# Performance work log

Hardware: AMD Instinct MI355X
Metric: run time of the kernel (lower is better)

Reference implementation:

```python
import jax, jax.numpy as jnp
import numpy as np

N = 20000      # nodes
E = 320000     # edges (before self-loops)
G = 64         # graphs in batch
H = 4          # attention heads
C = 64         # channels per head
HID = H * C    # 256
IN = 128       # input feature dim
LAT = 64       # latent dim
NEG = 0.2      # LeakyReLU negative slope (PyG GATConv default)
BN_EPS = 1e-5
N_LAYERS = 3


def setup_inputs() -> dict:
    key = jax.random.key(0)
    ks = jax.random.split(key, 24)
    s = 0.1
    return dict(
        x=jax.random.normal(ks[0], (N, IN), jnp.float32),
        edge_index=jax.random.randint(ks[1], (2, E), 0, N, dtype=jnp.int32),
        batch=jnp.sort(jax.random.randint(ks[2], (N,), 0, G, dtype=jnp.int32)),
        W0=jax.random.normal(ks[3], (IN, HID), jnp.float32) * s,
        W_rest=jax.random.normal(ks[4], (N_LAYERS - 1, HID, HID), jnp.float32) * s,
        att_src=jax.random.normal(ks[5], (N_LAYERS, H, C), jnp.float32) * s,
        att_dst=jax.random.normal(ks[6], (N_LAYERS, H, C), jnp.float32) * s,
        bias_conv=jax.random.normal(ks[7], (N_LAYERS, HID), jnp.float32) * s,
        bn_gamma=jax.random.uniform(ks[8], (N_LAYERS, HID), jnp.float32) + 0.5,
        bn_beta=jax.random.normal(ks[9], (N_LAYERS, HID), jnp.float32) * s,
        bn_mean=jax.random.normal(ks[10], (N_LAYERS, HID), jnp.float32) * s,
        bn_var=jax.random.uniform(ks[11], (N_LAYERS, HID), jnp.float32) + 0.5,
        lbn_gamma=jax.random.uniform(ks[12], (HID,), jnp.float32) + 0.5,
        lbn_beta=jax.random.normal(ks[13], (HID,), jnp.float32) * s,
        lbn_mean=jax.random.normal(ks[14], (HID,), jnp.float32) * s,
        lbn_var=jax.random.uniform(ks[15], (HID,), jnp.float32) + 0.5,
        fc_W=jax.random.normal(ks[16], (HID, LAT), jnp.float32) * s,
        fc_b=jax.random.normal(ks[17], (LAT,), jnp.float32) * s,
    )


def _gat_layer(x, src, dst, W, a_src, a_dst, bias):
    # linear transform -> [N, H, C]
    xp = (x @ W).reshape(N, H, C)
    # per-node attention scalars [N, H]
    al_s = (xp * a_src).sum(-1)
    al_d = (xp * a_dst).sum(-1)
    # per-edge logit for edge j->i: leaky_relu(a_s[j] + a_d[i])
    e = jax.nn.leaky_relu(al_s[src] + al_d[dst], NEG)  # [E', H]
    # softmax over incoming edges of each target node
    emax = jax.ops.segment_max(e, dst, num_segments=N)  # [N, H]
    ex = jnp.exp(e - emax[dst])
    denom = jax.ops.segment_sum(ex, dst, num_segments=N)
    alpha = ex / (denom[dst] + 1e-16)
    # weighted scatter-add of source features
    msg = xp[src] * alpha[:, :, None]                    # [E', H, C]
    out = jax.ops.segment_sum(msg, dst, num_segments=N)  # [N, H, C]
    return out.reshape(N, HID) + bias


def _bn_eval(x, gamma, beta, mean, var):
    return (x - mean) * jax.lax.rsqrt(var + BN_EPS) * gamma + beta


def reference(x, edge_index, batch, W0, W_rest, att_src, att_dst, bias_conv,
              bn_gamma, bn_beta, bn_mean, bn_var,
              lbn_gamma, lbn_beta, lbn_mean, lbn_var, fc_W, fc_b):
    # PyG convention: edge_index[0]=source, edge_index[1]=target; GATConv adds self-loops
    loop = jnp.arange(N, dtype=edge_index.dtype)
    src = jnp.concatenate([edge_index[0], loop])
    dst = jnp.concatenate([edge_index[1], loop])
    h = x
    for i in range(N_LAYERS):
        W = W0 if i == 0 else W_rest[i - 1]
        h = _gat_layer(h, src, dst, W, att_src[i], att_dst[i], bias_conv[i])
        h = _bn_eval(h, bn_gamma[i], bn_beta[i], bn_mean[i], bn_var[i])
        h = jax.nn.relu(h)
        # dropout is identity in eval mode
    pooled = jax.ops.segment_sum(h, batch, num_segments=G)  # [G, HID]
    pooled = _bn_eval(pooled, lbn_gamma, lbn_beta, lbn_mean, lbn_var)
    return pooled @ fc_W + fc_b  # [G, LAT]
```

## Files before the change

kernel.cpp:

```cpp
#include <hip/hip_runtime.h>
#include <hip/hip_bf16.h>
#include <cmath>

#define NN   20000
#define NE   320000
#define EE   (NE + NN)
#define NG   64
#define NH   4
#define NC   64
#define HIDD 256
#define IND  128
#define LATD 64
#define NEGS 0.2f
#define BNEPS 1e-5f
#define MPAD 20096
#define PSPLIT 16
#define NB   ((NN + 255) / 256)

#define BM 128
#define BN 64
#define BK 64

typedef __attribute__((ext_vector_type(8))) short short8;
typedef __attribute__((ext_vector_type(4))) float f32x4;

__device__ inline int lower_bound_i(const int* __restrict__ b, int n, int key) {
    int lo = 0, hi = n;
    while (lo < hi) { int mid = (lo + hi) >> 1; if (b[mid] < key) lo = mid + 1; else hi = mid; }
    return lo;
}

__device__ inline float sel4(float4 v, int h) {
    float r = v.x;
    r = (h == 1) ? v.y : r;
    r = (h == 2) ? v.z : r;
    r = (h == 3) ? v.w : r;
    return r;
}

__device__ inline float bf2f(unsigned short u) {
    return __uint_as_float(((unsigned int)u) << 16);
}

__global__ void k_zero(int* __restrict__ p, int n) {
    int i = blockIdx.x * blockDim.x + threadIdx.x;
    if (i < n) p[i] = 0;
}

__global__ void k_cast_x(const float* __restrict__ x, __hip_bfloat16* __restrict__ hbx) {
    int i = blockIdx.x * blockDim.x + threadIdx.x;
    if (i >= NN * IND / 4) return;
    float4 v = ((const float4*)x)[i];
    union { __hip_bfloat16 b[4]; ushort4 u; } cv;
    cv.b[0] = __float2bfloat16(v.x); cv.b[1] = __float2bfloat16(v.y);
    cv.b[2] = __float2bfloat16(v.z); cv.b[3] = __float2bfloat16(v.w);
    ((ushort4*)hbx)[i] = cv.u;
}

__global__ void k_cast_wt_all(const float* __restrict__ W0, const float* __restrict__ Wr,
                              __hip_bfloat16* __restrict__ Wt3) {
    int k = blockIdx.x;
    int l = blockIdx.y;
    int n = threadIdx.x;
    int K = (l == 0) ? IND : HIDD;
    if (k >= K) return;
    const float* W = (l == 0) ? W0 : (Wr + (size_t)(l - 1) * HIDD * HIDD);
    size_t off = (l == 0) ? 0 : ((size_t)HIDD * IND + (size_t)(l - 1) * HIDD * HIDD);
    Wt3[off + (size_t)n * K + k] = __float2bfloat16(W[(size_t)k * HIDD + n]);
}

__global__ void k_hist(const int* __restrict__ ei, int* __restrict__ deg) {
    int e = blockIdx.x * blockDim.x + threadIdx.x;
    if (e >= EE) return;
    int d = (e < NE) ? ei[NE + e] : (e - NE);
    atomicAdd(&deg[d], 1);
}

__global__ __launch_bounds__(256) void k_blocksum(const int* __restrict__ deg,
                                                  int* __restrict__ bsum) {
    __shared__ int s[256];
    int i = blockIdx.x * 256 + threadIdx.x;
    s[threadIdx.x] = (i < NN) ? deg[i] : 0;
    __syncthreads();
    for (int off = 128; off > 0; off >>= 1) {
        if (threadIdx.x < off) s[threadIdx.x] += s[threadIdx.x + off];
        __syncthreads();
    }
    if (threadIdx.x == 0) bsum[blockIdx.x] = s[0];
}

__global__ __launch_bounds__(128) void k_scanbs(const int* __restrict__ bsum,
                                                int* __restrict__ boff,
                                                int* __restrict__ row_ptr) {
    __shared__ int s[128];
    int tid = threadIdx.x;
    int v = (tid < NB) ? bsum[tid] : 0;
    s[tid] = v;
    __syncthreads();
    for (int off = 1; off < 128; off <<= 1) {
        int t = (tid >= off) ? s[tid - off] : 0;
        __syncthreads();
        s[tid] += t;
        __syncthreads();
    }
    if (tid < NB) boff[tid] = s[tid] - v;
    if (tid == NB - 1) row_ptr[NN] = s[tid];
}

__global__ __launch_bounds__(256) void k_scanapply(const int* __restrict__ deg,
                                                   const int* __restrict__ boff,
                                                   int* __restrict__ row_ptr,
                                                   int* __restrict__ cursor) {
    __shared__ int s[256];
    int i = blockIdx.x * 256 + threadIdx.x;
    int v = (i < NN) ? deg[i] : 0;
    s[threadIdx.x] = v;
    __syncthreads();
    for (int off = 1; off < 256; off <<= 1) {
        int t = (threadIdx.x >= off) ? s[threadIdx.x - off] : 0;
        __syncthreads();
        s[threadIdx.x] += t;
        __syncthreads();
    }
    if (i < NN) {
        int excl = boff[blockIdx.x] + s[threadIdx.x] - v;
        row_ptr[i] = excl; cursor[i] = excl;
    }
}

__global__ void k_csr_scatter(const int* __restrict__ ei, int* __restrict__ cursor,
                              int* __restrict__ col_idx) {
    int e = blockIdx.x * blockDim.x + threadIdx.x;
    if (e >= EE) return;
    int s, d;
    if (e < NE) { s = ei[e]; d = ei[NE + e]; } else { s = d = e - NE; }
    int pos = atomicAdd(&cursor[d], 1);
    col_idx[pos] = s;
}

__global__ __launch_bounds__(256) void k_gemm(const short* __restrict__ A,
                                              const short* __restrict__ Bt,
                                              int K, __hip_bfloat16* __restrict__ Cb,
                                              const float* __restrict__ a_src,
                                              const float* __restrict__ a_dst,
                                              float* __restrict__ al_s,
                                              float* __restrict__ al_d) {
    __shared__ char As[BM * BK * 2];
    __shared__ char Bs[BN * BK * 2];
    __shared__ float redS[2][BM];
    __shared__ float redD[2][BM];
    int tid = threadIdx.x;
    int lane = tid & 63;
    int wid = tid >> 6;
    int wm = wid >> 1, wn = wid & 1;
    int bm0 = blockIdx.x * BM, bn0 = blockIdx.y * BN;
    int r16 = lane & 15, kg = lane >> 4;

    f32x4 acc[4][2];
    #pragma unroll
    for (int m = 0; m < 4; ++m)
        #pragma unroll
        for (int n = 0; n < 2; ++n) acc[m][n] = (f32x4){0.f, 0.f, 0.f, 0.f};

    for (int k0 = 0; k0 < K; k0 += BK) {
        __syncthreads();
        #pragma unroll
        for (int p = 0; p < 4; ++p) {
            int row = p * 32 + (tid >> 3);
            int cg  = tid & 7;
            uint4 v = *(const uint4*)(A + (size_t)(bm0 + row) * K + k0 + cg * 8);
            *(uint4*)(As + row * 128 + ((cg * 16) ^ ((row & 7) << 4))) = v;
        }
        #pragma unroll
        for (int p = 0; p < 2; ++p) {
            int row = p * 32 + (tid >> 3);
            int cg  = tid & 7;
            uint4 v = *(const uint4*)(Bt + (size_t)(bn0 + row) * K + k0 + cg * 8);
            *(uint4*)(Bs + row * 128 + ((cg * 16) ^ ((row & 7) << 4))) = v;
        }
        __syncthreads();
        #pragma unroll
        for (int kk = 0; kk < 2; ++kk) {
            short8 af[4], bfr[2];
            int kb = (kk * 32 + kg * 8) * 2;
            #pragma unroll
            for (int m = 0; m < 4; ++m) {
                int row = wm * 64 + m * 16 + r16;
                af[m] = *(const short8*)(As + row * 128 + (kb ^ ((row & 7) << 4)));
            }
            #pragma unroll
            for (int n = 0; n < 2; ++n) {
                int row = wn * 32 + n * 16 + r16;
                bfr[n] = *(const short8*)(Bs + row * 128 + (kb ^ ((row & 7) << 4)));
            }
            #pragma unroll
            for (int m = 0; m < 4; ++m)
                #pragma unroll
                for (int n = 0; n < 2; ++n)
                    acc[m][n] = __builtin_amdgcn_mfma_f32_16x16x32_bf16(af[m], bfr[n], acc[m][n], 0, 0, 0);
        }
    }

    #pragma unroll
    for (int m = 0; m < 4; ++m) {
        int row = bm0 + wm * 64 + m * 16 + kg * 4;
        #pragma unroll
        for (int n = 0; n < 2; ++n) {
            int col = bn0 + wn * 32 + n * 16 + r16;
            #pragma unroll
            for (int r = 0; r < 4; ++r)
                Cb[(size_t)(row + r) * HIDD + col] = __float2bfloat16(acc[m][n][r]);
        }
    }

    int headbase = bn0;
    float as0 = a_src[headbase + wn * 32 + r16];
    float as1 = a_src[headbase + wn * 32 + 16 + r16];
    float ad0 = a_dst[headbase + wn * 32 + r16];
    float ad1 = a_dst[headbase + wn * 32 + 16 + r16];
    #pragma unroll
    for (int m = 0; m < 4; ++m) {
        #pragma unroll
        for (int r = 0; r < 4; ++r) {
            float ps = as0 * acc[m][0][r] + as1 * acc[m][1][r];
            float pd = ad0 * acc[m][0][r] + ad1 * acc[m][1][r];
            #pragma unroll
            for (int msk = 1; msk < 16; msk <<= 1) {
                ps += __shfl_xor(ps, msk, 64);
                pd += __shfl_xor(pd, msk, 64);
            }
            if (r16 == 0) {
                int rl = wm * 64 + m * 16 + kg * 4 + r;
                redS[wn][rl] = ps;
                redD[wn][rl] = pd;
            }
        }
    }
    __syncthreads();
    if (tid < BM) {
        int node = bm0 + tid;
        al_s[node * NH + blockIdx.y] = redS[0][tid] + redS[1][tid];
        al_d[node * NH + blockIdx.y] = redD[0][tid] + redD[1][tid];
    }
}

#define EDGE_BODY(I) \
    { float l = as##I + adh; l = l > 0.f ? l : NEGS * l; \
      float wt = __expf(l); den##I += wt; \
      acc##I.x = fmaf(wt, bf2f(xv##I.x), acc##I.x); \
      acc##I.y = fmaf(wt, bf2f(xv##I.y), acc##I.y); \
      acc##I.z = fmaf(wt, bf2f(xv##I.z), acc##I.z); \
      acc##I.w = fmaf(wt, bf2f(xv##I.w), acc##I.w); }

__global__ __launch_bounds__(256) void k_gat_agg(
        const int* __restrict__ row_ptr, const int* __restrict__ col_idx,
        const float* __restrict__ al_s, const float* __restrict__ al_d,
        const __hip_bfloat16* __restrict__ xpb,
        const float* __restrict__ bias, const float* __restrict__ bg,
        const float* __restrict__ bb, const float* __restrict__ bm,
        const float* __restrict__ bv,
        float* __restrict__ h, __hip_bfloat16* __restrict__ hb, int wmask) {
    int wid = threadIdx.x >> 6, lane = threadIdx.x & 63;
    int node = blockIdx.x * 4 + wid;
    if (node >= NN) return;
    int lo = row_ptr[node], hi = row_ptr[node + 1];
    int hsel = lane >> 4;
    float adh = sel4(((const float4*)al_d)[node], hsel);

    float4 acc0 = {0,0,0,0}, acc1 = {0,0,0,0}, acc2 = {0,0,0,0}, acc3 = {0,0,0,0};
    float den0 = 0.f, den1 = 0.f, den2 = 0.f, den3 = 0.f;

    int e = lo;
    for (; e + 3 < hi; e += 4) {
        int sc0 = col_idx[e], sc1 = col_idx[e + 1], sc2 = col_idx[e + 2], sc3 = col_idx[e + 3];
        float as0 = al_s[sc0 * NH + hsel];
        float as1 = al_s[sc1 * NH + hsel];
        float as2 = al_s[sc2 * NH + hsel];
        float as3 = al_s[sc3 * NH + hsel];
        ushort4 xv0 = ((const ushort4*)(xpb + (size_t)sc0 * HIDD))[lane];
        ushort4 xv1 = ((const ushort4*)(xpb + (size_t)sc1 * HIDD))[lane];
        ushort4 xv2 = ((const ushort4*)(xpb + (size_t)sc2 * HIDD))[lane];
        ushort4 xv3 = ((const ushort4*)(xpb + (size_t)sc3 * HIDD))[lane];
        EDGE_BODY(0) EDGE_BODY(1) EDGE_BODY(2) EDGE_BODY(3)
    }
    for (; e < hi; ++e) {
        int sc0 = col_idx[e];
        float as0 = al_s[sc0 * NH + hsel];
        ushort4 xv0 = ((const ushort4*)(xpb + (size_t)sc0 * HIDD))[lane];
        EDGE_BODY(0)
    }

    float den = (den0 + den1) + (den2 + den3);
    float inv = 1.f / (den + 1e-16f);
    float4 acc;
    acc.x = ((acc0.x + acc1.x) + (acc2.x + acc3.x)) * inv;
    acc.y = ((acc0.y + acc1.y) + (acc2.y + acc3.y)) * inv;
    acc.z = ((acc0.z + acc1.z) + (acc2.z + acc3.z)) * inv;
    acc.w = ((acc0.w + acc1.w) + (acc2.w + acc3.w)) * inv;

    float4 bi = ((const float4*)bias)[lane];
    float4 gg = ((const float4*)bg)[lane];
    float4 be = ((const float4*)bb)[lane];
    float4 mn = ((const float4*)bm)[lane];
    float4 vr = ((const float4*)bv)[lane];
    float4 val;
    val.x = (acc.x + bi.x - mn.x) * rsqrtf(vr.x + BNEPS) * gg.x + be.x;
    val.y = (acc.y + bi.y - mn.y) * rsqrtf(vr.y + BNEPS) * gg.y + be.y;
    val.z = (acc.z + bi.z - mn.z) * rsqrtf(vr.z + BNEPS) * gg.z + be.z;
    val.w = (acc.w + bi.w - mn.w) * rsqrtf(vr.w + BNEPS) * gg.w + be.w;
    val.x = val.x > 0.f ? val.x : 0.f;
    val.y = val.y > 0.f ? val.y : 0.f;
    val.z = val.z > 0.f ? val.z : 0.f;
    val.w = val.w > 0.f ? val.w : 0.f;
    if (wmask & 1)
        ((float4*)h)[(size_t)node * 64 + lane] = val;
    if (wmask & 2) {
        union { __hip_bfloat16 b[4]; ushort4 u; } cv;
        cv.b[0] = __float2bfloat16(val.x); cv.b[1] = __float2bfloat16(val.y);
        cv.b[2] = __float2bfloat16(val.z); cv.b[3] = __float2bfloat16(val.w);
        ((ushort4*)hb)[(size_t)node * 64 + lane] = cv.u;
    }
}

__global__ void k_pool2(const float* __restrict__ h, const int* __restrict__ batch,
                        float* __restrict__ partial) {
    int g = blockIdx.x, i = blockIdx.y, col = threadIdx.x;
    int lo = lower_bound_i(batch, NN, g);
    int hi = lower_bound_i(batch, NN, g + 1);
    int len = hi - lo;
    int a = lo + (int)((long)len * i / PSPLIT);
    int b = lo + (int)((long)len * (i + 1) / PSPLIT);
    float acc = 0.f;
    for (int n = a; n < b; ++n) acc += h[(size_t)n * HIDD + col];
    partial[((size_t)g * PSPLIT + i) * HIDD + col] = acc;
}

__global__ __launch_bounds__(64) void k_final(const float* __restrict__ partial,
                                              const float* __restrict__ lg,
                                              const float* __restrict__ lb,
                                              const float* __restrict__ lm,
                                              const float* __restrict__ lv,
                                              const float* __restrict__ fcW,
                                              const float* __restrict__ fcb,
                                              float* __restrict__ out) {
    __shared__ float ps[HIDD];
    int g = blockIdx.x, j = threadIdx.x;
    for (int k = j; k < HIDD; k += 64) {
        float s = 0.f;
        for (int i = 0; i < PSPLIT; ++i)
            s += partial[((size_t)g * PSPLIT + i) * HIDD + k];
        ps[k] = (s - lm[k]) * rsqrtf(lv[k] + BNEPS) * lg[k] + lb[k];
    }
    __syncthreads();
    float acc = 0.f;
    for (int k = 0; k < HIDD; ++k)
        acc = fmaf(ps[k], fcW[k * LATD + j], acc);
    out[g * LATD + j] = acc + fcb[j];
}

extern "C" void kernel_launch(void* const* d_in, const int* in_sizes, int n_in,
                              void* d_out, int out_size, void* d_ws, size_t ws_size,
                              hipStream_t stream) {
    const float* x     = (const float*)d_in[0];
    const int*   ei    = (const int*)d_in[1];
    const int*   batch = (const int*)d_in[2];
    const float* W0    = (const float*)d_in[3];
    const float* Wr    = (const float*)d_in[4];
    const float* asrc  = (const float*)d_in[5];
    const float* adst  = (const float*)d_in[6];
    const float* bconv = (const float*)d_in[7];
    const float* bng   = (const float*)d_in[8];
    const float* bnb   = (const float*)d_in[9];
    const float* bnm   = (const float*)d_in[10];
    const float* bnv   = (const float*)d_in[11];
    const float* lg    = (const float*)d_in[12];
    const float* lb    = (const float*)d_in[13];
    const float* lm    = (const float*)d_in[14];
    const float* lv    = (const float*)d_in[15];
    const float* fcW   = (const float*)d_in[16];
    const float* fcb   = (const float*)d_in[17];
    float* out = (float*)d_out;

    char* w = (char*)d_ws;
    size_t off = 0;
    auto alloc = [&](size_t bytes) {
        char* p = w + off;
        off += (bytes + 255) / 256 * 256;
        return p;
    };
    float* hbuf  = (float*)alloc((size_t)NN * HIDD * 4);
    float* al_s  = (float*)alloc((size_t)MPAD * NH * 4);
    float* al_d  = (float*)alloc((size_t)MPAD * NH * 4);
    float* partial = (float*)alloc((size_t)NG * PSPLIT * HIDD * 4);
    __hip_bfloat16* hbx = (__hip_bfloat16*)alloc((size_t)MPAD * IND * 2);
    __hip_bfloat16* hb2 = (__hip_bfloat16*)alloc((size_t)MPAD * HIDD * 2);
    __hip_bfloat16* xpb = (__hip_bfloat16*)alloc((size_t)MPAD * HIDD * 2);
    __hip_bfloat16* Wt3 = (__hip_bfloat16*)alloc(((size_t)HIDD * IND + 2 * (size_t)HIDD * HIDD) * 2);
    int* deg     = (int*)alloc((size_t)NN * 4);
    int* row_ptr = (int*)alloc((size_t)(NN + 1) * 4);
    int* cursor  = (int*)alloc((size_t)NN * 4);
    int* col_idx = (int*)alloc((size_t)EE * 4);
    int* bsum    = (int*)alloc((size_t)NB * 4);
    int* boff    = (int*)alloc((size_t)NB * 4);

    hipLaunchKernelGGL(k_zero, dim3(NB), dim3(256), 0, stream, deg, NN);
    hipLaunchKernelGGL(k_hist, dim3((EE + 255) / 256), dim3(256), 0, stream, ei, deg);
    hipLaunchKernelGGL(k_blocksum, dim3(NB), dim3(256), 0, stream, deg, bsum);
    hipLaunchKernelGGL(k_scanbs, dim3(1), dim3(128), 0, stream, bsum, boff, row_ptr);
    hipLaunchKernelGGL(k_scanapply, dim3(NB), dim3(256), 0, stream, deg, boff, row_ptr, cursor);
    hipLaunchKernelGGL(k_csr_scatter, dim3((EE + 255) / 256), dim3(256), 0, stream,
                       ei, cursor, col_idx);

    hipLaunchKernelGGL(k_cast_x, dim3((NN * IND / 4 + 255) / 256), dim3(256), 0, stream, x, hbx);
    hipLaunchKernelGGL(k_cast_wt_all, dim3(HIDD, 3), dim3(HIDD), 0, stream, W0, Wr, Wt3);

    const size_t wtoff[3] = {0, (size_t)HIDD * IND, (size_t)HIDD * IND + (size_t)HIDD * HIDD};

    for (int layer = 0; layer < 3; ++layer) {
        int K = (layer == 0) ? IND : HIDD;
        const __hip_bfloat16* Ab = (layer == 0) ? hbx : hb2;
        int wmask = (layer == 2) ? 1 : 2;

        hipLaunchKernelGGL(k_gemm, dim3(MPAD / BM, HIDD / BN), dim3(256), 0, stream,
                           (const short*)Ab, (const short*)(Wt3 + wtoff[layer]), K, xpb,
                           asrc + layer * NH * NC, adst + layer * NH * NC, al_s, al_d);
        hipLaunchKernelGGL(k_gat_agg, dim3((NN + 3) / 4), dim3(256), 0, stream,
                           row_ptr, col_idx, al_s, al_d, xpb,
                           bconv + layer * HIDD, bng + layer * HIDD, bnb + layer * HIDD,
                           bnm + layer * HIDD, bnv + layer * HIDD, hbuf, hb2, wmask);
    }

    hipLaunchKernelGGL(k_pool2, dim3(NG, PSPLIT), dim3(HIDD), 0, stream, hbuf, batch, partial);
    hipLaunchKernelGGL(k_final, dim3(NG), dim3(LATD), 0, stream,
                       partial, lg, lb, lm, lv, fcW, fcb, out);
}
```

Measured before the change: 208.0 us.

## Split projected features into two column slices for cache-resident gather aggregation

The GEMM now writes the projected bf16 features as two column slices of 128 channels, each stored contiguously. Aggregation then runs as two launches, one per slice, so each pass gathers from a 5 MB working set that fits better in L2/MALL instead of the full 10 MB. The final layer also writes bf16 instead of fp32, and pooling reads bf16, dropping the fp32 hidden buffer. This costs a second pass over the CSR indices and the attention logits and recomputes the exp weights in each slice, and the bf16 pooling input slightly lowers precision.

```diff
diff --git a/kernel.cpp b/kernel.cpp
--- a/kernel.cpp
+++ b/kernel.cpp
@@ -207,9 +207,10 @@
         #pragma unroll
         for (int n = 0; n < 2; ++n) {
             int col = bn0 + wn * 32 + n * 16 + r16;
+            size_t base = (size_t)(col >> 7) * MPAD * 128 + (col & 127);
             #pragma unroll
             for (int r = 0; r < 4; ++r)
-                Cb[(size_t)(row + r) * HIDD + col] = __float2bfloat16(acc[m][n][r]);
+                Cb[base + (size_t)(row + r) * 128] = __float2bfloat16(acc[m][n][r]);
         }
     }
 
@@ -247,27 +248,26 @@
 #define EDGE_BODY(I) \
     { float l = as##I + adh; l = l > 0.f ? l : NEGS * l; \
       float wt = __expf(l); den##I += wt; \
-      acc##I.x = fmaf(wt, bf2f(xv##I.x), acc##I.x); \
-      acc##I.y = fmaf(wt, bf2f(xv##I.y), acc##I.y); \
-      acc##I.z = fmaf(wt, bf2f(xv##I.z), acc##I.z); \
-      acc##I.w = fmaf(wt, bf2f(xv##I.w), acc##I.w); }
-
-__global__ __launch_bounds__(256) void k_gat_agg(
+      acc##I.x = fmaf(wt, bf2f((unsigned short)(xv##I & 0xffffu)), acc##I.x); \
+      acc##I.y = fmaf(wt, bf2f((unsigned short)(xv##I >> 16)), acc##I.y); }
+
+__global__ __launch_bounds__(256) void k_gat_agg2(
         const int* __restrict__ row_ptr, const int* __restrict__ col_idx,
         const float* __restrict__ al_s, const float* __restrict__ al_d,
-        const __hip_bfloat16* __restrict__ xpb,
+        const __hip_bfloat16* __restrict__ xps,
         const float* __restrict__ bias, const float* __restrict__ bg,
         const float* __restrict__ bb, const float* __restrict__ bm,
         const float* __restrict__ bv,
-        float* __restrict__ h, __hip_bfloat16* __restrict__ hb, int wmask) {
+        __hip_bfloat16* __restrict__ hb, int slice) {
     int wid = threadIdx.x >> 6, lane = threadIdx.x & 63;
     int node = blockIdx.x * 4 + wid;
     if (node >= NN) return;
     int lo = row_ptr[node], hi = row_ptr[node + 1];
-    int hsel = lane >> 4;
+    int gc = slice * 128 + lane * 2;
+    int hsel = gc >> 6;
     float adh = sel4(((const float4*)al_d)[node], hsel);
 
-    float4 acc0 = {0,0,0,0}, acc1 = {0,0,0,0}, acc2 = {0,0,0,0}, acc3 = {0,0,0,0};
+    float2 acc0 = {0,0}, acc1 = {0,0}, acc2 = {0,0}, acc3 = {0,0};
     float den0 = 0.f, den1 = 0.f, den2 = 0.f, den3 = 0.f;
 
     int e = lo;
@@ -277,52 +277,40 @@
         float as1 = al_s[sc1 * NH + hsel];
         float as2 = al_s[sc2 * NH + hsel];
         float as3 = al_s[sc3 * NH + hsel];
-        ushort4 xv0 = ((const ushort4*)(xpb + (size_t)sc0 * HIDD))[lane];
-        ushort4 xv1 = ((const ushort4*)(xpb + (size_t)sc1 * HIDD))[lane];
-        ushort4 xv2 = ((const ushort4*)(xpb + (size_t)sc2 * HIDD))[lane];
-        ushort4 xv3 = ((const ushort4*)(xpb + (size_t)sc3 * HIDD))[lane];
+        unsigned int xv0 = *(const unsigned int*)(xps + (size_t)sc0 * 128 + lane * 2);
+        unsigned int xv1 = *(const unsigned int*)(xps + (size_t)sc1 * 128 + lane * 2);
+        unsigned int xv2 = *(const unsigned int*)(xps + (size_t)sc2 * 128 + lane * 2);
+        unsigned int xv3 = *(const unsigned int*)(xps + (size_t)sc3 * 128 + lane * 2);
         EDGE_BODY(0) EDGE_BODY(1) EDGE_BODY(2) EDGE_BODY(3)
     }
     for (; e < hi; ++e) {
         int sc0 = col_idx[e];
         float as0 = al_s[sc0 * NH + hsel];
-        ushort4 xv0 = ((const ushort4*)(xpb + (size_t)sc0 * HIDD))[lane];
+        unsigned int xv0 = *(const unsigned int*)(xps + (size_t)sc0 * 128 + lane * 2);
         EDGE_BODY(0)
     }
 
     float den = (den0 + den1) + (den2 + den3);
     float inv = 1.f / (den + 1e-16f);
-    float4 acc;
+    float2 acc;
     acc.x = ((acc0.x + acc1.x) + (acc2.x + acc3.x)) * inv;
     acc.y = ((acc0.y + acc1.y) + (acc2.y + acc3.y)) * inv;
-    acc.z = ((acc0.z + acc1.z) + (acc2.z + acc3.z)) * inv;
-    acc.w = ((acc0.w + acc1.w) + (acc2.w + acc3.w)) * inv;
-
-    float4 bi = ((const float4*)bias)[lane];
-    float4 gg = ((const float4*)bg)[lane];
-    float4 be = ((const float4*)bb)[lane];
-    float4 mn = ((const float4*)bm)[lane];
-    float4 vr = ((const float4*)bv)[lane];
-    float4 val;
-    val.x = (acc.x + bi.x - mn.x) * rsqrtf(vr.x + BNEPS) * gg.x + be.x;
-    val.y = (acc.y + bi.y - mn.y) * rsqrtf(vr.y + BNEPS) * gg.y + be.y;
-    val.z = (acc.z + bi.z - mn.z) * rsqrtf(vr.z + BNEPS) * gg.z + be.z;
-    val.w = (acc.w + bi.w - mn.w) * rsqrtf(vr.w + BNEPS) * gg.w + be.w;
-    val.x = val.x > 0.f ? val.x : 0.f;
-    val.y = val.y > 0.f ? val.y : 0.f;
-    val.z = val.z > 0.f ? val.z : 0.f;
-    val.w = val.w > 0.f ? val.w : 0.f;
-    if (wmask & 1)
-        ((float4*)h)[(size_t)node * 64 + lane] = val;
-    if (wmask & 2) {
-        union { __hip_bfloat16 b[4]; ushort4 u; } cv;
-        cv.b[0] = __float2bfloat16(val.x); cv.b[1] = __float2bfloat16(val.y);
-        cv.b[2] = __float2bfloat16(val.z); cv.b[3] = __float2bfloat16(val.w);
-        ((ushort4*)hb)[(size_t)node * 64 + lane] = cv.u;
-    }
-}
-
-__global__ void k_pool2(const float* __restrict__ h, const int* __restrict__ batch,
+
+    float2 bi = *(const float2*)(bias + gc);
+    float2 gg = *(const float2*)(bg + gc);
+    float2 be = *(const float2*)(bb + gc);
+    float2 mn = *(const float2*)(bm + gc);
+    float2 vr = *(const float2*)(bv + gc);
+    float vx = (acc.x + bi.x - mn.x) * rsqrtf(vr.x + BNEPS) * gg.x + be.x;
+    float vy = (acc.y + bi.y - mn.y) * rsqrtf(vr.y + BNEPS) * gg.y + be.y;
+    vx = vx > 0.f ? vx : 0.f;
+    vy = vy > 0.f ? vy : 0.f;
+    union { __hip_bfloat16 b[2]; unsigned int u; } cv;
+    cv.b[0] = __float2bfloat16(vx); cv.b[1] = __float2bfloat16(vy);
+    *(unsigned int*)((unsigned short*)hb + (size_t)node * HIDD + gc) = cv.u;
+}
+
+__global__ void k_pool2(const __hip_bfloat16* __restrict__ hb, const int* __restrict__ batch,
                         float* __restrict__ partial) {
     int g = blockIdx.x, i = blockIdx.y, col = threadIdx.x;
     int lo = lower_bound_i(batch, NN, g);
@@ -331,7 +319,8 @@
     int a = lo + (int)((long)len * i / PSPLIT);
     int b = lo + (int)((long)len * (i + 1) / PSPLIT);
     float acc = 0.f;
-    for (int n = a; n < b; ++n) acc += h[(size_t)n * HIDD + col];
+    const unsigned short* hu = (const unsigned short*)hb;
+    for (int n = a; n < b; ++n) acc += bf2f(hu[(size_t)n * HIDD + col]);
     partial[((size_t)g * PSPLIT + i) * HIDD + col] = acc;
 }
 
@@ -388,13 +377,12 @@
         off += (bytes + 255) / 256 * 256;
         return p;
     };
-    float* hbuf  = (float*)alloc((size_t)NN * HIDD * 4);
     float* al_s  = (float*)alloc((size_t)MPAD * NH * 4);
     float* al_d  = (float*)alloc((size_t)MPAD * NH * 4);
     float* partial = (float*)alloc((size_t)NG * PSPLIT * HIDD * 4);
     __hip_bfloat16* hbx = (__hip_bfloat16*)alloc((size_t)MPAD * IND * 2);
     __hip_bfloat16* hb2 = (__hip_bfloat16*)alloc((size_t)MPAD * HIDD * 2);
-    __hip_bfloat16* xpb = (__hip_bfloat16*)alloc((size_t)MPAD * HIDD * 2);
+    __hip_bfloat16* xpb2 = (__hip_bfloat16*)alloc((size_t)2 * MPAD * 128 * 2);
     __hip_bfloat16* Wt3 = (__hip_bfloat16*)alloc(((size_t)HIDD * IND + 2 * (size_t)HIDD * HIDD) * 2);
     int* deg     = (int*)alloc((size_t)NN * 4);
     int* row_ptr = (int*)alloc((size_t)(NN + 1) * 4);
@@ -419,18 +407,20 @@
     for (int layer = 0; layer < 3; ++layer) {
         int K = (layer == 0) ? IND : HIDD;
         const __hip_bfloat16* Ab = (layer == 0) ? hbx : hb2;
-        int wmask = (layer == 2) ? 1 : 2;
 
         hipLaunchKernelGGL(k_gemm, dim3(MPAD / BM, HIDD / BN), dim3(256), 0, stream,
-                           (const short*)Ab, (const short*)(Wt3 + wtoff[layer]), K, xpb,
+                           (const short*)Ab, (const short*)(Wt3 + wtoff[layer]), K, xpb2,
                            asrc + layer * NH * NC, adst + layer * NH * NC, al_s, al_d);
-        hipLaunchKernelGGL(k_gat_agg, dim3((NN + 3) / 4), dim3(256), 0, stream,
-                           row_ptr, col_idx, al_s, al_d, xpb,
-                           bconv + layer * HIDD, bng + layer * HIDD, bnb + layer * HIDD,
-                           bnm + layer * HIDD, bnv + layer * HIDD, hbuf, hb2, wmask);
-    }
-
-    hipLaunchKernelGGL(k_pool2, dim3(NG, PSPLIT), dim3(HIDD), 0, stream, hbuf, batch, partial);
+        for (int slice = 0; slice < 2; ++slice) {
+            hipLaunchKernelGGL(k_gat_agg2, dim3((NN + 3) / 4), dim3(256), 0, stream,
+                               row_ptr, col_idx, al_s, al_d,
+                               xpb2 + (size_t)slice * MPAD * 128,
+                               bconv + layer * HIDD, bng + layer * HIDD, bnb + layer * HIDD,
+                               bnm + layer * HIDD, bnv + layer * HIDD, hb2, slice);
+        }
+    }
+
+    hipLaunchKernelGGL(k_pool2, dim3(NG, PSPLIT), dim3(HIDD), 0, stream, hb2, batch, partial);
     hipLaunchKernelGGL(k_final, dim3(NG), dim3(LATD), 0, stream,
                        partial, lg, lb, lm, lv, fcW, fcb, out);
 }
```

After: 244.6 us. 17.6% more time.
